# Kernel optimization log

Measured on AMD Instinct MI355X. Metric: run time of the kernel, lower is better.

## Reference

```python
import jax, jax.numpy as jnp
import numpy as np

B, S, HID, NH = 2, 2048, 2048, 16
NOPE, ROPE, VD = 128, 64, 128
QKD = NOPE + ROPE          # 192
KVR, QR = 512, 1536
EPS = 1e-6
SCALE = QKD ** (-0.5)


def rmsnorm(x, gamma, eps=EPS):
    return x * jax.lax.rsqrt(jnp.mean(x * x, axis=-1, keepdims=True) + eps) * gamma


def rotate_half(x):
    h = x.shape[-1] // 2
    return jnp.concatenate([-x[..., h:], x[..., :h]], axis=-1)


def apply_rope(x, cos, sin):
    # x: [b, h, s, d_rope]; cos/sin: [b, 1, s, d_rope]
    return x * cos + rotate_half(x) * sin


def setup_inputs() -> dict:
    key = jax.random.key(0)
    ks = jax.random.split(key, 8)
    hidden_states = jax.random.normal(ks[0], (B, S, HID), dtype=jnp.float32)
    # Standard NeoX-style rotary tables for the decoupled RoPE sub-dim
    pos = jnp.arange(S, dtype=jnp.float32)
    inv_freq = 1.0 / (10000.0 ** (jnp.arange(0, ROPE, 2, dtype=jnp.float32) / ROPE))
    freqs = pos[:, None] * inv_freq[None, :]              # [S, ROPE/2]
    emb = jnp.concatenate([freqs, freqs], axis=-1)        # [S, ROPE]
    cos = jnp.broadcast_to(jnp.cos(emb)[None], (B, S, ROPE)).astype(jnp.float32)
    sin = jnp.broadcast_to(jnp.sin(emb)[None], (B, S, ROPE)).astype(jnp.float32)
    std = 0.02
    Wq_down = jax.random.normal(ks[1], (QR, HID), dtype=jnp.float32) * std
    q_gamma = jnp.ones((QR,), dtype=jnp.float32)
    Wq_up = jax.random.normal(ks[2], (NH * QKD, QR), dtype=jnp.float32) * std
    Wkv_down = jax.random.normal(ks[3], (KVR + ROPE, HID), dtype=jnp.float32) * std
    kv_gamma = jnp.ones((KVR,), dtype=jnp.float32)
    Wkv_up = jax.random.normal(ks[4], (NH * (NOPE + VD), KVR), dtype=jnp.float32) * std
    Wo = jax.random.normal(ks[5], (HID, NH * VD), dtype=jnp.float32) * std
    return {
        "hidden_states": hidden_states, "cos": cos, "sin": sin,
        "Wq_down": Wq_down, "q_gamma": q_gamma, "Wq_up": Wq_up,
        "Wkv_down": Wkv_down, "kv_gamma": kv_gamma, "Wkv_up": Wkv_up,
        "Wo": Wo,
    }


def reference(hidden_states, cos, sin, Wq_down, q_gamma, Wq_up,
              Wkv_down, kv_gamma, Wkv_up, Wo):
    b, s, _ = hidden_states.shape
    cos4 = cos[:, None, :, :]  # [b,1,s,ROPE]
    sin4 = sin[:, None, :, :]

    # Q path: low-rank down -> RMSNorm -> up
    q_lat = rmsnorm(hidden_states @ Wq_down.T, q_gamma)            # [b,s,QR]
    q = (q_lat @ Wq_up.T).reshape(b, s, NH, QKD).transpose(0, 2, 1, 3)  # [b,h,s,QKD]
    q_nope, q_rope = q[..., :NOPE], q[..., NOPE:]
    q_rope = apply_rope(q_rope, cos4, sin4)
    q = jnp.concatenate([q_nope, q_rope], axis=-1)                 # [b,h,s,QKD]

    # KV path: joint down-proj -> split latent / shared rope key
    kv = hidden_states @ Wkv_down.T                                # [b,s,KVR+ROPE]
    c_kv, k_rope = kv[..., :KVR], kv[..., KVR:]
    c_kv = rmsnorm(c_kv, kv_gamma)
    kvx = (c_kv @ Wkv_up.T).reshape(b, s, NH, NOPE + VD).transpose(0, 2, 1, 3)
    k_nope, v = kvx[..., :NOPE], kvx[..., NOPE:]                   # [b,h,s,*]

    # Shared rope key, broadcast to all heads, rotated
    k_rope = apply_rope(k_rope[:, None, :, :], cos4, sin4)         # [b,1,s,ROPE]
    k_rope = jnp.broadcast_to(k_rope, (b, NH, s, ROPE))
    k = jnp.concatenate([k_nope, k_rope], axis=-1)                 # [b,h,s,QKD]

    # SDPA with causal mask (V zero-padded to QKD in the original -> identical
    # to using V directly and slicing, so we use V directly)
    scores = jnp.einsum('bhqd,bhkd->bhqk', q, k) * SCALE           # [b,h,s,s]
    causal = jnp.tril(jnp.ones((s, s), dtype=bool))
    scores = jnp.where(causal[None, None], scores, jnp.finfo(scores.dtype).min)
    attn = jax.nn.softmax(scores, axis=-1)
    out = jnp.einsum('bhqk,bhkd->bhqd', attn, v)                   # [b,h,s,VD]
    out = out.transpose(0, 2, 1, 3).reshape(b, s, NH * VD)
    return out @ Wo.T                                              # [b,s,HID]
```

## Files before the change

kernel.cpp:

```cpp
#include <hip/hip_runtime.h>
#include <math.h>

#define SCALE_F 0.0721687836487032f

typedef __attribute__((ext_vector_type(8))) short bf16x8;
typedef __attribute__((ext_vector_type(4))) float f32x4;
typedef __attribute__((ext_vector_type(4))) unsigned short u16x4;

static __device__ __forceinline__ short f2bf(float f) {
  unsigned u = __float_as_uint(f);
  u += 0x7fffu + ((u >> 16) & 1u);
  return (short)(u >> 16);
}

static __device__ __forceinline__ void gl_lds16(const void* g, void* l) {
  __builtin_amdgcn_global_load_lds((const __attribute__((address_space(1))) void*)g,
                                   (__attribute__((address_space(3))) void*)l, 16, 0, 0);
}

template <int MODE>
__global__ __launch_bounds__(256) void gemm_mfma(
    const short* __restrict__ A, const short* __restrict__ W,
    void* __restrict__ Cout, int N, int K,
    const float* __restrict__ cosb, const float* __restrict__ sinb,
    short* __restrict__ out2)
{
  __shared__ __align__(16) short As[128 * 32];
  __shared__ __align__(16) short Ws[128 * 32];
  const int tid = threadIdx.x;
  const int lane = tid & 63;
  const int quad = lane >> 4, n16 = lane & 15;
  const int bm = blockIdx.y * 128, bn = blockIdx.x * 128;
  const int wr = ((tid >> 6) >> 1) * 64, wc = ((tid >> 6) & 1) * 64;

  f32x4 acc[4][4];
  #pragma unroll
  for (int i = 0; i < 4; ++i)
    #pragma unroll
    for (int j = 0; j < 4; ++j) acc[i][j] = (f32x4){0.f, 0.f, 0.f, 0.f};

  const int r0 = tid >> 2, c0 = (tid & 3) * 8;
  const short* a0p = A + (size_t)(bm + r0) * K + c0;
  const short* a1p = A + (size_t)(bm + 64 + r0) * K + c0;
  const short* w0p = W + (size_t)(bn + r0) * K + c0;
  const short* w1p = W + (size_t)(bn + 64 + r0) * K + c0;
  short* asd0 = &As[tid * 8];
  short* asd1 = &As[2048 + tid * 8];
  short* wsd0 = &Ws[tid * 8];
  short* wsd1 = &Ws[2048 + tid * 8];

  for (int k0 = 0; k0 < K; k0 += 32) {
    gl_lds16(a0p, asd0);
    gl_lds16(a1p, asd1);
    gl_lds16(w0p, wsd0);
    gl_lds16(w1p, wsd1);
    a0p += 32; a1p += 32; w0p += 32; w1p += 32;
    __syncthreads();

    bf16x8 af[4], wf[4];
    #pragma unroll
    for (int i = 0; i < 4; ++i) {
      af[i] = *(const bf16x8*)&As[(wr + i * 16 + n16) * 32 + quad * 8];
      wf[i] = *(const bf16x8*)&Ws[(wc + i * 16 + n16) * 32 + quad * 8];
    }
    #pragma unroll
    for (int i = 0; i < 4; ++i)
      #pragma unroll
      for (int j = 0; j < 4; ++j)
        acc[i][j] = __builtin_amdgcn_mfma_f32_16x16x32_bf16(af[i], wf[j], acc[i][j], 0, 0, 0);
    __syncthreads();
  }

  if (MODE == 0) {
    #pragma unroll
    for (int i = 0; i < 4; ++i)
      #pragma unroll
      for (int r = 0; r < 4; ++r) {
        size_t row = (size_t)(bm + wr + i * 16 + quad * 4 + r);
        #pragma unroll
        for (int j = 0; j < 4; ++j)
          ((float*)Cout)[row * N + bn + wc + j * 16 + n16] = acc[i][j][r];
      }
  } else if (MODE == 2) {
    #pragma unroll
    for (int i = 0; i < 4; ++i)
      #pragma unroll
      for (int r = 0; r < 4; ++r) {
        int m = bm + wr + i * 16 + quad * 4 + r;
        int bb = m >> 11, s = m & 2047;
        #pragma unroll
        for (int j = 0; j < 4; ++j) {
          int col = bn + wc + j * 16 + n16;
          int h = col / 192, c = col - h * 192;
          float v = acc[i][j][r];
          if (c >= 128) {
            int jr = c - 128;
            float part = acc[i][j ^ 2][r];
            float cs = cosb[(size_t)m * 64 + jr], sn = sinb[(size_t)m * 64 + jr];
            v = (jr < 32) ? (v * cs - part * sn) : (v * cs + part * sn);
          }
          ((short*)Cout)[(((size_t)(bb * 16 + h)) * 2048 + s) * 192 + c] = f2bf(v * SCALE_F);
        }
      }
  } else {
    #pragma unroll
    for (int i = 0; i < 4; ++i)
      #pragma unroll
      for (int r = 0; r < 4; ++r) {
        int m = bm + wr + i * 16 + quad * 4 + r;
        int bb = m >> 11, s = m & 2047;
        #pragma unroll
        for (int j = 0; j < 4; ++j) {
          int col = bn + wc + j * 16 + n16;
          int h = col >> 8, c = col & 255;
          short v = f2bf(acc[i][j][r]);
          if (c < 128)
            ((short*)Cout)[(((size_t)(bb * 16 + h)) * 2048 + s) * 192 + c] = v;
          else
            out2[((size_t)(bb * 16 + h) * 128 + (c - 128)) * 2048 + s] = v;
        }
      }
  }
}

__global__ __launch_bounds__(256) void cast_all(
    const float* __restrict__ hidden, const float* __restrict__ Wqd,
    const float* __restrict__ Wqu, const float* __restrict__ Wkvu,
    const float* __restrict__ Wo, const float* __restrict__ Wkvd,
    short* __restrict__ hb, short* __restrict__ Wqd_b, short* __restrict__ Wqu_b,
    short* __restrict__ Wkvu_b, short* __restrict__ Wo_b, short* __restrict__ Wkvd_b)
{
  int blk = blockIdx.x;
  const float* src; short* dst; int i;
  if (blk < 8192)       { src = hidden; dst = hb;     i = (blk * 256 + threadIdx.x) * 4; }
  else if (blk < 11264) { src = Wqd;  dst = Wqd_b;  i = ((blk - 8192) * 256 + threadIdx.x) * 4; }
  else if (blk < 15872) { src = Wqu;  dst = Wqu_b;  i = ((blk - 11264) * 256 + threadIdx.x) * 4; }
  else if (blk < 17920) { src = Wkvu; dst = Wkvu_b; i = ((blk - 15872) * 256 + threadIdx.x) * 4; }
  else if (blk < 22016) { src = Wo;   dst = Wo_b;   i = ((blk - 17920) * 256 + threadIdx.x) * 4; }
  else {
    i = ((blk - 22016) * 256 + threadIdx.x) * 4;
    int r = i >> 11;
    short4 o = {0, 0, 0, 0};
    if (r < 576) {
      float4 v = *(const float4*)(Wkvd + i);
      o.x = f2bf(v.x); o.y = f2bf(v.y); o.z = f2bf(v.z); o.w = f2bf(v.w);
    }
    *(short4*)(Wkvd_b + i) = o;
    return;
  }
  float4 v = *(const float4*)(src + i);
  short4 o = { f2bf(v.x), f2bf(v.y), f2bf(v.z), f2bf(v.w) };
  *(short4*)(dst + i) = o;
}

__global__ __launch_bounds__(256) void rmsnorm_cast(
    const float* __restrict__ X, const float* __restrict__ gamma,
    short* __restrict__ Y, int C, int sx, int sy)
{
  const float* x = X + (size_t)blockIdx.x * sx;
  short* y = Y + (size_t)blockIdx.x * sy;
  const int tid = threadIdx.x;
  float ss = 0.f;
  for (int c = tid * 4; c < C; c += 1024) {
    float4 v = *(const float4*)(x + c);
    ss += v.x * v.x + v.y * v.y + v.z * v.z + v.w * v.w;
  }
  #pragma unroll
  for (int off = 32; off > 0; off >>= 1) ss += __shfl_down(ss, off, 64);
  __shared__ float red[4];
  if ((tid & 63) == 0) red[tid >> 6] = ss;
  __syncthreads();
  float tot = red[0] + red[1] + red[2] + red[3];
  float scale = rsqrtf(tot / (float)C + 1e-6f);
  for (int c = tid * 4; c < C; c += 1024) {
    float4 v = *(const float4*)(x + c);
    float4 g = *(const float4*)(gamma + c);
    short4 o = { f2bf(v.x * scale * g.x), f2bf(v.y * scale * g.y),
                 f2bf(v.z * scale * g.z), f2bf(v.w * scale * g.w) };
    *(short4*)(y + c) = o;
  }
}

__global__ __launch_bounds__(256) void rmsnorm_kv_rope(
    const float* __restrict__ kvf, const float* __restrict__ gamma,
    const float* __restrict__ cosb, const float* __restrict__ sinb,
    short* __restrict__ ckv, short* __restrict__ kr)
{
  const int m = blockIdx.x;
  const float* x = kvf + (size_t)m * 640;
  short* y = ckv + (size_t)m * 512;
  const int tid = threadIdx.x;
  float ss = 0.f;
  for (int c = tid * 4; c < 512; c += 1024) {
    float4 v = *(const float4*)(x + c);
    ss += v.x * v.x + v.y * v.y + v.z * v.z + v.w * v.w;
  }
  #pragma unroll
  for (int off = 32; off > 0; off >>= 1) ss += __shfl_down(ss, off, 64);
  __shared__ float red[4];
  if ((tid & 63) == 0) red[tid >> 6] = ss;
  __syncthreads();
  float tot = red[0] + red[1] + red[2] + red[3];
  float scale = rsqrtf(tot / 512.f + 1e-6f);
  for (int c = tid * 4; c < 512; c += 1024) {
    float4 v = *(const float4*)(x + c);
    float4 g = *(const float4*)(gamma + c);
    short4 o = { f2bf(v.x * scale * g.x), f2bf(v.y * scale * g.y),
                 f2bf(v.z * scale * g.z), f2bf(v.w * scale * g.w) };
    *(short4*)(y + c) = o;
  }
  if (tid < 32) {
    const float* cb = cosb + (size_t)m * 64;
    const float* sb = sinb + (size_t)m * 64;
    float x1 = x[512 + tid], x2 = x[512 + tid + 32];
    kr[(size_t)m * 64 + tid]      = f2bf(x1 * cb[tid] - x2 * sb[tid]);
    kr[(size_t)m * 64 + tid + 32] = f2bf(x2 * cb[tid + 32] + x1 * sb[tid + 32]);
  }
}

__global__ __launch_bounds__(256) void krope_fill(
    const short* __restrict__ kr, short* __restrict__ Kb)
{
  int m = blockIdx.x;
  int b = m >> 11, s = m & 2047;
  for (int idx = threadIdx.x; idx < 1024; idx += 256) {
    int h = idx >> 6, j = idx & 63;
    Kb[(((size_t)(b * 16 + h)) * 2048 + s) * 192 + 128 + j] = kr[(size_t)m * 64 + j];
  }
}

#define PSTR 72

__global__ __launch_bounds__(512) void flash_mfma(
    const short* __restrict__ Qb, const short* __restrict__ Kb,
    const short* __restrict__ Vt, short* __restrict__ attnb)
{
  __shared__ __align__(16) short KVs[2][40 * 512];
  __shared__ __align__(16) short Ps[8][32 * PSTR];

  const int h = blockIdx.x;
  const int p = blockIdx.y;
  const int b = blockIdx.z;
  const int bh = b * 16 + h;
  const int tid = threadIdx.x;
  const int wave = tid >> 6, lane = tid & 63;
  const int grp = wave >> 2, w4 = wave & 3;
  const int quad = lane >> 4, n16 = lane & 15;
  const int lq = lane >> 2, lr = lane & 3;
  const int qt_h = 15 - p;
  const int L = 2 * p + 2;
  const int NIT = 17;

  int qw = (grp ? p : qt_h) * 128 + w4 * 32;

  const short* kS[6]; short* kD[6];
  #pragma unroll
  for (int u = 0; u < 6; ++u) {
    kS[u] = Kb + ((size_t)bh * 2048 + w4 * 16 + lq) * 192 + u * 32 + lr * 8;
    kD[u] = &KVs[grp][(w4 * 6 + u) * 512 + lane * 8];
  }
  const short* vS[4]; short* vD[4];
  #pragma unroll
  for (int u = 0; u < 4; ++u) {
    int ci = w4 * 4 + u, ks = ci >> 3, vt = ci & 7;
    vS[u] = Vt + ((size_t)bh * 128 + vt * 16 + lq) * 2048 + ks * 32 + lr * 8;
    vD[u] = &KVs[grp][(24 + ci) * 512 + lane * 8];
  }

  bf16x8 aQ[2][6];
  #pragma unroll
  for (int rg = 0; rg < 2; ++rg) {
    const short* qp = Qb + ((size_t)bh * 2048 + qw + rg * 16 + n16) * 192 + quad * 8;
    #pragma unroll
    for (int t = 0; t < 6; ++t) aQ[rg][t] = *(const bf16x8*)(qp + t * 32);
  }

  f32x4 O[2][8];
  #pragma unroll
  for (int rg = 0; rg < 2; ++rg)
    #pragma unroll
    for (int i = 0; i < 8; ++i) O[rg][i] = (f32x4){0.f, 0.f, 0.f, 0.f};
  float lp[2] = {0.f, 0.f};

  short* pw = &Ps[wave][0];

  {
    #pragma unroll
    for (int u = 0; u < 6; ++u) gl_lds16(kS[u], kD[u]);
    #pragma unroll
    for (int u = 0; u < 4; ++u) gl_lds16(vS[u], vD[u]);
  }

  for (int j = 0; j < NIT; ++j) {
    __syncthreads();

    if (grp == 1 && j == L) {
      #pragma unroll
      for (int rg = 0; rg < 2; ++rg) {
        float l = lp[rg];
        l += __shfl_xor(l, 16);
        l += __shfl_xor(l, 32);
        float inv_l[4];
        #pragma unroll
        for (int r = 0; r < 4; ++r) inv_l[r] = 1.f / __shfl(l, quad * 4 + r);
        #pragma unroll
        for (int vt = 0; vt < 8; ++vt)
          #pragma unroll
          for (int r = 0; r < 4; ++r) {
            size_t m = (size_t)b * 2048 + qw + rg * 16 + quad * 4 + r;
            attnb[(m * 16 + h) * 128 + vt * 16 + n16] = f2bf(O[rg][vt][r] * inv_l[r]);
          }
      }
      #pragma unroll
      for (int rg = 0; rg < 2; ++rg)
        #pragma unroll
        for (int i = 0; i < 8; ++i) O[rg][i] = (f32x4){0.f, 0.f, 0.f, 0.f};
      lp[0] = 0.f; lp[1] = 0.f;
      qw = qt_h * 128 + w4 * 32;
      #pragma unroll
      for (int rg = 0; rg < 2; ++rg) {
        const short* qp = Qb + ((size_t)bh * 2048 + qw + rg * 16 + n16) * 192 + quad * 8;
        #pragma unroll
        for (int t = 0; t < 6; ++t) aQ[rg][t] = *(const bf16x8*)(qp + t * 32);
      }
    }

    const int kt = (grp == 0) ? j : (j < L ? j : 17 + j - L);

    if (kt * 64 <= qw + 31) {
      float s[4][2][4];
      bool act[4];
      const bool tail = (kt * 64 + 63 > qw);
      #pragma unroll
      for (int ct = 0; ct < 4; ++ct) {
        act[ct] = (kt * 64 + ct * 16 <= qw + 31);
        if (act[ct]) {
          f32x4 a0 = (f32x4){0.f, 0.f, 0.f, 0.f};
          f32x4 a1 = (f32x4){0.f, 0.f, 0.f, 0.f};
          #pragma unroll
          for (int t = 0; t < 6; ++t) {
            bf16x8 ak = *(const bf16x8*)&KVs[grp][(ct * 6 + t) * 512 + n16 * 32 + quad * 8];
            a0 = __builtin_amdgcn_mfma_f32_16x16x32_bf16(ak, aQ[0][t], a0, 0, 0, 0);
            a1 = __builtin_amdgcn_mfma_f32_16x16x32_bf16(ak, aQ[1][t], a1, 0, 0, 0);
          }
          #pragma unroll
          for (int r = 0; r < 4; ++r) { s[ct][0][r] = a0[r]; s[ct][1][r] = a1[r]; }
        }
      }

      #pragma unroll
      for (int rg = 0; rg < 2; ++rg) {
        const int q = qw + rg * 16 + n16;
        #pragma unroll
        for (int ct = 0; ct < 4; ++ct) {
          u16x4 pk;
          #pragma unroll
          for (int r = 0; r < 4; ++r) {
            float v = 0.f;
            if (act[ct]) {
              v = __expf(s[ct][rg][r]);
              if (tail) {
                int key = kt * 64 + ct * 16 + quad * 4 + r;
                if (key > q) v = 0.f;
              }
            }
            lp[rg] += v;
            pk[r] = (unsigned short)f2bf(v);
          }
          *(u16x4*)&pw[(rg * 16 + n16) * PSTR + ct * 16 + quad * 4] = pk;
        }
      }

      #pragma unroll
      for (int ks = 0; ks < 2; ++ks) {
        if (kt * 64 + ks * 32 <= qw + 31) {
          bf16x8 aP0 = *(const bf16x8*)&pw[(n16) * PSTR + ks * 32 + quad * 8];
          bf16x8 aP1 = *(const bf16x8*)&pw[(16 + n16) * PSTR + ks * 32 + quad * 8];
          #pragma unroll
          for (int vt = 0; vt < 8; ++vt) {
            bf16x8 bV = *(const bf16x8*)&KVs[grp][(24 + ks * 8 + vt) * 512 + n16 * 32 + quad * 8];
            O[0][vt] = __builtin_amdgcn_mfma_f32_16x16x32_bf16(aP0, bV, O[0][vt], 0, 0, 0);
            O[1][vt] = __builtin_amdgcn_mfma_f32_16x16x32_bf16(aP1, bV, O[1][vt], 0, 0, 0);
          }
        }
      }
    }

    __syncthreads();

    if (j + 1 < NIT) {
      const int jn = j + 1;
      const int ktn = (grp == 0) ? jn : (jn < L ? jn : 17 + jn - L);
      const size_t ka = (size_t)ktn * (64 * 192);
      const size_t va = (size_t)ktn * 64;
      #pragma unroll
      for (int u = 0; u < 6; ++u) gl_lds16(kS[u] + ka, kD[u]);
      #pragma unroll
      for (int u = 0; u < 4; ++u) gl_lds16(vS[u] + va, vD[u]);
    }
  }

  float* xO = (float*)&KVs[0][0];
  float* xl = (float*)&Ps[0][0];
  const int xb = w4 * 4160 + lane * 65;
  if (grp == 1) {
    #pragma unroll
    for (int rg = 0; rg < 2; ++rg)
      #pragma unroll
      for (int vt = 0; vt < 8; ++vt)
        #pragma unroll
        for (int r = 0; r < 4; ++r)
          xO[xb + rg * 32 + vt * 4 + r] = O[rg][vt][r];
    xl[w4 * 128 + lane * 2 + 0] = lp[0];
    xl[w4 * 128 + lane * 2 + 1] = lp[1];
  }
  __syncthreads();
  if (grp == 0) {
    #pragma unroll
    for (int rg = 0; rg < 2; ++rg)
      #pragma unroll
      for (int vt = 0; vt < 8; ++vt)
        #pragma unroll
        for (int r = 0; r < 4; ++r)
          O[rg][vt][r] += xO[xb + rg * 32 + vt * 4 + r];
    lp[0] += xl[w4 * 128 + lane * 2 + 0];
    lp[1] += xl[w4 * 128 + lane * 2 + 1];

    #pragma unroll
    for (int rg = 0; rg < 2; ++rg) {
      float l = lp[rg];
      l += __shfl_xor(l, 16);
      l += __shfl_xor(l, 32);
      float inv_l[4];
      #pragma unroll
      for (int r = 0; r < 4; ++r) inv_l[r] = 1.f / __shfl(l, quad * 4 + r);
      #pragma unroll
      for (int vt = 0; vt < 8; ++vt)
        #pragma unroll
        for (int r = 0; r < 4; ++r) {
          size_t m = (size_t)b * 2048 + qw + rg * 16 + quad * 4 + r;
          attnb[(m * 16 + h) * 128 + vt * 16 + n16] = f2bf(O[rg][vt][r] * inv_l[r]);
        }
    }
  }
}

extern "C" void kernel_launch(void* const* d_in, const int* in_sizes, int n_in,
                              void* d_out, int out_size, void* d_ws, size_t ws_size,
                              hipStream_t stream)
{
  const float* hidden   = (const float*)d_in[0];
  const float* cosb     = (const float*)d_in[1];
  const float* sinb     = (const float*)d_in[2];
  const float* Wq_down  = (const float*)d_in[3];
  const float* q_gamma  = (const float*)d_in[4];
  const float* Wq_up    = (const float*)d_in[5];
  const float* Wkv_down = (const float*)d_in[6];
  const float* kv_gamma = (const float*)d_in[7];
  const float* Wkv_up   = (const float*)d_in[8];
  const float* Wo       = (const float*)d_in[9];
  float* out = (float*)d_out;

  char* base = (char*)d_ws;
  short* hb  = (short*)base;
  float* kvf = (float*)(base + 16777216);
  short* Qb  = (short*)base;
  char* pB = base + 27262976;
  short* Wqd_b  = (short*)pB;
  short* Wkvd_b = (short*)(pB + 6291456);
  short* Wqu_b  = (short*)(pB + 8912896);
  short* Wkvu_b = (short*)(pB + 18350080);
  short* Wo_b   = (short*)(pB + 22544384);
  char* pC = pB + 30932992;
  float* q_lat = (float*)pC;
  short* Kb    = (short*)pC;
  char* pD = pC + 25165824;
  short* q_lat_b = (short*)pD;
  short* ckv_b   = (short*)(pD + 12582912);
  short* krope_b = (short*)(pD + 16777216);
  short* attn_b  = (short*)pD;
  char* pE = pD + 17301504;
  short* Vt = (short*)pE;

  dim3 blk(256);

  cast_all<<<23296, blk, 0, stream>>>(hidden, Wq_down, Wq_up, Wkv_up, Wo, Wkv_down,
                                      hb, Wqd_b, Wqu_b, Wkvu_b, Wo_b, Wkvd_b);

  gemm_mfma<0><<<dim3(12, 32), blk, 0, stream>>>(hb, Wqd_b, q_lat, 1536, 2048, nullptr, nullptr, nullptr);
  gemm_mfma<0><<<dim3(5, 32), blk, 0, stream>>>(hb, Wkvd_b, kvf, 640, 2048, nullptr, nullptr, nullptr);

  rmsnorm_cast<<<4096, blk, 0, stream>>>(q_lat, q_gamma, q_lat_b, 1536, 1536, 1536);
  rmsnorm_kv_rope<<<4096, blk, 0, stream>>>(kvf, kv_gamma, cosb, sinb, ckv_b, krope_b);

  gemm_mfma<2><<<dim3(24, 32), blk, 0, stream>>>(q_lat_b, Wqu_b, Qb, 3072, 1536, cosb, sinb, nullptr);
  gemm_mfma<3><<<dim3(32, 32), blk, 0, stream>>>(ckv_b, Wkvu_b, Kb, 4096, 512, nullptr, nullptr, Vt);
  krope_fill<<<4096, blk, 0, stream>>>(krope_b, Kb);

  flash_mfma<<<dim3(16, 8, 2), dim3(512), 0, stream>>>(Qb, Kb, Vt, attn_b);
  gemm_mfma<0><<<dim3(16, 32), blk, 0, stream>>>(attn_b, Wo_b, out, 2048, 2048, nullptr, nullptr, nullptr);
}
```

Measured before the change: 515.1 us.

## Merge Q/KV down and up projection GEMMs into single launches, transpose V via LDS

Fuses the Q-down and KV-down projections into one GEMM launch over a concatenated N of 2176, splitting the output by column range. It also merges the Q-up and KV-up GEMMs into one kernel that picks its operands by block index, which fills the GPU better and removes launch gaps. The V half of the KV-up output is now transposed through LDS and written with 16-byte row stores instead of scattered 2-byte stores. The merged down GEMM assumes the bf16 Wq_down and Wkv_down buffers sit next to each other in memory. The extra LDS transpose buffer raises shared-memory use and may lower occupancy.

After: 576.0 us. 11.8% more time.

```diff
diff --git a/kernel.cpp b/kernel.cpp
--- a/kernel.cpp
+++ b/kernel.cpp
@@ -81,7 +81,86 @@
         for (int j = 0; j < 4; ++j)
           ((float*)Cout)[row * N + bn + wc + j * 16 + n16] = acc[i][j][r];
       }
-  } else if (MODE == 2) {
+  } else {
+    float* qlat = (float*)Cout;
+    float* kvf  = (float*)out2;
+    #pragma unroll
+    for (int i = 0; i < 4; ++i)
+      #pragma unroll
+      for (int r = 0; r < 4; ++r) {
+        size_t row = (size_t)(bm + wr + i * 16 + quad * 4 + r);
+        #pragma unroll
+        for (int j = 0; j < 4; ++j) {
+          int col = bn + wc + j * 16 + n16;
+          if (col < 1536) qlat[row * 1536 + col] = acc[i][j][r];
+          else            kvf[row * 640 + (col - 1536)] = acc[i][j][r];
+        }
+      }
+  }
+}
+
+__global__ __launch_bounds__(256) void gemm_up(
+    const short* __restrict__ Aq, const short* __restrict__ Wq,
+    short* __restrict__ Qb,
+    const float* __restrict__ cosb, const float* __restrict__ sinb,
+    const short* __restrict__ Akv, const short* __restrict__ Wkv,
+    short* __restrict__ Kb, short* __restrict__ Vtb)
+{
+  __shared__ __align__(16) short As[128 * 32];
+  __shared__ __align__(16) short Ws[128 * 32];
+  __shared__ __align__(16) short Tt[128 * 136];
+
+  const bool isQ = blockIdx.x < 24;
+  const short* A = isQ ? Aq : Akv;
+  const short* W = isQ ? Wq : Wkv;
+  const int K = isQ ? 1536 : 512;
+  const int bx = isQ ? blockIdx.x : (blockIdx.x - 24);
+
+  const int tid = threadIdx.x;
+  const int lane = tid & 63;
+  const int quad = lane >> 4, n16 = lane & 15;
+  const int bm = blockIdx.y * 128, bn = bx * 128;
+  const int wr = ((tid >> 6) >> 1) * 64, wc = ((tid >> 6) & 1) * 64;
+
+  f32x4 acc[4][4];
+  #pragma unroll
+  for (int i = 0; i < 4; ++i)
+    #pragma unroll
+    for (int j = 0; j < 4; ++j) acc[i][j] = (f32x4){0.f, 0.f, 0.f, 0.f};
+
+  const int r0 = tid >> 2, c0 = (tid & 3) * 8;
+  const short* a0p = A + (size_t)(bm + r0) * K + c0;
+  const short* a1p = A + (size_t)(bm + 64 + r0) * K + c0;
+  const short* w0p = W + (size_t)(bn + r0) * K + c0;
+  const short* w1p = W + (size_t)(bn + 64 + r0) * K + c0;
+  short* asd0 = &As[tid * 8];
+  short* asd1 = &As[2048 + tid * 8];
+  short* wsd0 = &Ws[tid * 8];
+  short* wsd1 = &Ws[2048 + tid * 8];
+
+  for (int k0 = 0; k0 < K; k0 += 32) {
+    gl_lds16(a0p, asd0);
+    gl_lds16(a1p, asd1);
+    gl_lds16(w0p, wsd0);
+    gl_lds16(w1p, wsd1);
+    a0p += 32; a1p += 32; w0p += 32; w1p += 32;
+    __syncthreads();
+
+    bf16x8 af[4], wf[4];
+    #pragma unroll
+    for (int i = 0; i < 4; ++i) {
+      af[i] = *(const bf16x8*)&As[(wr + i * 16 + n16) * 32 + quad * 8];
+      wf[i] = *(const bf16x8*)&Ws[(wc + i * 16 + n16) * 32 + quad * 8];
+    }
+    #pragma unroll
+    for (int i = 0; i < 4; ++i)
+      #pragma unroll
+      for (int j = 0; j < 4; ++j)
+        acc[i][j] = __builtin_amdgcn_mfma_f32_16x16x32_bf16(af[i], wf[j], acc[i][j], 0, 0, 0);
+    __syncthreads();
+  }
+
+  if (isQ) {
     #pragma unroll
     for (int i = 0; i < 4; ++i)
       #pragma unroll
@@ -99,10 +178,11 @@
             float cs = cosb[(size_t)m * 64 + jr], sn = sinb[(size_t)m * 64 + jr];
             v = (jr < 32) ? (v * cs - part * sn) : (v * cs + part * sn);
           }
-          ((short*)Cout)[(((size_t)(bb * 16 + h)) * 2048 + s) * 192 + c] = f2bf(v * SCALE_F);
-        }
-      }
-  } else {
+          Qb[(((size_t)(bb * 16 + h)) * 2048 + s) * 192 + c] = f2bf(v * SCALE_F);
+        }
+      }
+  } else if ((bn & 255) == 0) {
+    const int h = bn >> 8;
     #pragma unroll
     for (int i = 0; i < 4; ++i)
       #pragma unroll
@@ -111,15 +191,29 @@
         int bb = m >> 11, s = m & 2047;
         #pragma unroll
         for (int j = 0; j < 4; ++j) {
-          int col = bn + wc + j * 16 + n16;
-          int h = col >> 8, c = col & 255;
-          short v = f2bf(acc[i][j][r]);
-          if (c < 128)
-            ((short*)Cout)[(((size_t)(bb * 16 + h)) * 2048 + s) * 192 + c] = v;
-          else
-            out2[((size_t)(bb * 16 + h) * 128 + (c - 128)) * 2048 + s] = v;
-        }
-      }
+          int c = wc + j * 16 + n16;
+          Kb[(((size_t)(bb * 16 + h)) * 2048 + s) * 192 + c] = f2bf(acc[i][j][r]);
+        }
+      }
+  } else {
+    const int h = bn >> 8;
+    #pragma unroll
+    for (int i = 0; i < 4; ++i)
+      #pragma unroll
+      for (int j = 0; j < 4; ++j) {
+        u16x4 pk;
+        #pragma unroll
+        for (int r = 0; r < 4; ++r) pk[r] = (unsigned short)f2bf(acc[i][j][r]);
+        *(u16x4*)&Tt[(wc + j * 16 + n16) * 136 + wr + i * 16 + quad * 4] = pk;
+      }
+    __syncthreads();
+    const int bb2 = bm >> 11, sb = bm & 2047;
+    const int cr = tid >> 1, hf = tid & 1;
+    const short* srcr = &Tt[cr * 136 + hf * 64];
+    short* dstr = Vtb + ((size_t)(bb2 * 16 + h) * 128 + cr) * 2048 + sb + hf * 64;
+    #pragma unroll
+    for (int k = 0; k < 8; ++k)
+      *(bf16x8*)(dstr + k * 8) = *(const bf16x8*)(srcr + k * 8);
   }
 }
 
@@ -487,16 +581,17 @@
   cast_all<<<23296, blk, 0, stream>>>(hidden, Wq_down, Wq_up, Wkv_up, Wo, Wkv_down,
                                       hb, Wqd_b, Wqu_b, Wkvu_b, Wo_b, Wkvd_b);
 
-  gemm_mfma<0><<<dim3(12, 32), blk, 0, stream>>>(hb, Wqd_b, q_lat, 1536, 2048, nullptr, nullptr, nullptr);
-  gemm_mfma<0><<<dim3(5, 32), blk, 0, stream>>>(hb, Wkvd_b, kvf, 640, 2048, nullptr, nullptr, nullptr);
+  gemm_mfma<4><<<dim3(17, 32), blk, 0, stream>>>(hb, Wqd_b, q_lat, 2176, 2048,
+                                                 nullptr, nullptr, (short*)kvf);
 
   rmsnorm_cast<<<4096, blk, 0, stream>>>(q_lat, q_gamma, q_lat_b, 1536, 1536, 1536);
   rmsnorm_kv_rope<<<4096, blk, 0, stream>>>(kvf, kv_gamma, cosb, sinb, ckv_b, krope_b);
 
-  gemm_mfma<2><<<dim3(24, 32), blk, 0, stream>>>(q_lat_b, Wqu_b, Qb, 3072, 1536, cosb, sinb, nullptr);
-  gemm_mfma<3><<<dim3(32, 32), blk, 0, stream>>>(ckv_b, Wkvu_b, Kb, 4096, 512, nullptr, nullptr, Vt);
+  gemm_up<<<dim3(56, 32), blk, 0, stream>>>(q_lat_b, Wqu_b, Qb, cosb, sinb,
+                                            ckv_b, Wkvu_b, Kb, Vt);
   krope_fill<<<4096, blk, 0, stream>>>(krope_b, Kb);
 
   flash_mfma<<<dim3(16, 8, 2), dim3(512), 0, stream>>>(Qb, Kb, Vt, attn_b);
-  gemm_mfma<0><<<dim3(16, 32), blk, 0, stream>>>(attn_b, Wo_b, out, 2048, 2048, nullptr, nullptr, nullptr);
-}
+  gemm_mfma<0><<<dim3(16, 32), blk, 0, stream>>>(attn_b, Wo_b, out, 2048, 2048,
+                                                 nullptr, nullptr, nullptr);
+}
```

## Fuse down-projection GEMMs, merge RMSNorm kernels, fold krope fill into KV-up epilogue

Applied to the files above, without the earlier changes.

Merges the Q and KV down-projection GEMMs into one launch over a concatenated weight (N=2176), with a new epilogue mode that splits columns into q_lat and kvf. Combines the two RMSNorm kernels into one launch, and folds the per-head rope-key broadcast into the MODE 3 GEMM epilogue so the separate krope_fill kernel is removed. Separately, the flash QK^T inner loop is split into two independent accumulator chains to shorten MFMA dependency chains. Fewer launches and better wave fill come at the cost of relying on Wqd_b and Wkvd_b being contiguous in memory, and of reusing the sinb pointer to pass krope.

New measurement: 479.1 us. -7.0%, faster.

```diff
diff --git a/kernel.cpp b/kernel.cpp
--- a/kernel.cpp
+++ b/kernel.cpp
@@ -102,7 +102,7 @@
           ((short*)Cout)[(((size_t)(bb * 16 + h)) * 2048 + s) * 192 + c] = f2bf(v * SCALE_F);
         }
       }
-  } else {
+  } else if (MODE == 3) {
     #pragma unroll
     for (int i = 0; i < 4; ++i)
       #pragma unroll
@@ -118,6 +118,32 @@
             ((short*)Cout)[(((size_t)(bb * 16 + h)) * 2048 + s) * 192 + c] = v;
           else
             out2[((size_t)(bb * 16 + h) * 128 + (c - 128)) * 2048 + s] = v;
+        }
+      }
+    if ((bn & 255) == 0) {
+      const short* kr = (const short*)sinb;
+      const int h = bn >> 8;
+      const int bb = bm >> 11, sb = bm & 2047;
+      const int rr = tid >> 1, half = tid & 1;
+      const short* src = kr + (size_t)(bm + rr) * 64 + half * 32;
+      short* dst = (short*)Cout + (((size_t)(bb * 16 + h)) * 2048 + sb + rr) * 192 + 128 + half * 32;
+      #pragma unroll
+      for (int k = 0; k < 4; ++k)
+        *(bf16x8*)(dst + k * 8) = *(const bf16x8*)(src + k * 8);
+    }
+  } else {
+    float* qlat = (float*)Cout;
+    float* kvf  = (float*)out2;
+    #pragma unroll
+    for (int i = 0; i < 4; ++i)
+      #pragma unroll
+      for (int r = 0; r < 4; ++r) {
+        size_t row = (size_t)(bm + wr + i * 16 + quad * 4 + r);
+        #pragma unroll
+        for (int j = 0; j < 4; ++j) {
+          int col = bn + wc + j * 16 + n16;
+          if (col < 1536) qlat[row * 1536 + col] = acc[i][j][r];
+          else            kvf[row * 640 + (col - 1536)] = acc[i][j][r];
         }
       }
   }
@@ -153,79 +179,66 @@
   *(short4*)(dst + i) = o;
 }
 
-__global__ __launch_bounds__(256) void rmsnorm_cast(
-    const float* __restrict__ X, const float* __restrict__ gamma,
-    short* __restrict__ Y, int C, int sx, int sy)
-{
-  const float* x = X + (size_t)blockIdx.x * sx;
-  short* y = Y + (size_t)blockIdx.x * sy;
-  const int tid = threadIdx.x;
-  float ss = 0.f;
-  for (int c = tid * 4; c < C; c += 1024) {
-    float4 v = *(const float4*)(x + c);
-    ss += v.x * v.x + v.y * v.y + v.z * v.z + v.w * v.w;
-  }
-  #pragma unroll
-  for (int off = 32; off > 0; off >>= 1) ss += __shfl_down(ss, off, 64);
-  __shared__ float red[4];
-  if ((tid & 63) == 0) red[tid >> 6] = ss;
-  __syncthreads();
-  float tot = red[0] + red[1] + red[2] + red[3];
-  float scale = rsqrtf(tot / (float)C + 1e-6f);
-  for (int c = tid * 4; c < C; c += 1024) {
-    float4 v = *(const float4*)(x + c);
-    float4 g = *(const float4*)(gamma + c);
-    short4 o = { f2bf(v.x * scale * g.x), f2bf(v.y * scale * g.y),
-                 f2bf(v.z * scale * g.z), f2bf(v.w * scale * g.w) };
-    *(short4*)(y + c) = o;
-  }
-}
-
-__global__ __launch_bounds__(256) void rmsnorm_kv_rope(
-    const float* __restrict__ kvf, const float* __restrict__ gamma,
+__global__ __launch_bounds__(256) void rmsnorm_both(
+    const float* __restrict__ q_lat, const float* __restrict__ q_gamma,
+    short* __restrict__ q_lat_b,
+    const float* __restrict__ kvf, const float* __restrict__ kv_gamma,
     const float* __restrict__ cosb, const float* __restrict__ sinb,
     short* __restrict__ ckv, short* __restrict__ kr)
 {
-  const int m = blockIdx.x;
-  const float* x = kvf + (size_t)m * 640;
-  short* y = ckv + (size_t)m * 512;
   const int tid = threadIdx.x;
-  float ss = 0.f;
-  for (int c = tid * 4; c < 512; c += 1024) {
-    float4 v = *(const float4*)(x + c);
-    ss += v.x * v.x + v.y * v.y + v.z * v.z + v.w * v.w;
-  }
-  #pragma unroll
-  for (int off = 32; off > 0; off >>= 1) ss += __shfl_down(ss, off, 64);
   __shared__ float red[4];
-  if ((tid & 63) == 0) red[tid >> 6] = ss;
-  __syncthreads();
-  float tot = red[0] + red[1] + red[2] + red[3];
-  float scale = rsqrtf(tot / 512.f + 1e-6f);
-  for (int c = tid * 4; c < 512; c += 1024) {
-    float4 v = *(const float4*)(x + c);
-    float4 g = *(const float4*)(gamma + c);
-    short4 o = { f2bf(v.x * scale * g.x), f2bf(v.y * scale * g.y),
-                 f2bf(v.z * scale * g.z), f2bf(v.w * scale * g.w) };
-    *(short4*)(y + c) = o;
-  }
-  if (tid < 32) {
-    const float* cb = cosb + (size_t)m * 64;
-    const float* sb = sinb + (size_t)m * 64;
-    float x1 = x[512 + tid], x2 = x[512 + tid + 32];
-    kr[(size_t)m * 64 + tid]      = f2bf(x1 * cb[tid] - x2 * sb[tid]);
-    kr[(size_t)m * 64 + tid + 32] = f2bf(x2 * cb[tid + 32] + x1 * sb[tid + 32]);
-  }
-}
-
-__global__ __launch_bounds__(256) void krope_fill(
-    const short* __restrict__ kr, short* __restrict__ Kb)
-{
-  int m = blockIdx.x;
-  int b = m >> 11, s = m & 2047;
-  for (int idx = threadIdx.x; idx < 1024; idx += 256) {
-    int h = idx >> 6, j = idx & 63;
-    Kb[(((size_t)(b * 16 + h)) * 2048 + s) * 192 + 128 + j] = kr[(size_t)m * 64 + j];
+  if (blockIdx.x < 4096) {
+    const int m = blockIdx.x;
+    const float* x = q_lat + (size_t)m * 1536;
+    short* y = q_lat_b + (size_t)m * 1536;
+    float ss = 0.f;
+    for (int c = tid * 4; c < 1536; c += 1024) {
+      float4 v = *(const float4*)(x + c);
+      ss += v.x * v.x + v.y * v.y + v.z * v.z + v.w * v.w;
+    }
+    #pragma unroll
+    for (int off = 32; off > 0; off >>= 1) ss += __shfl_down(ss, off, 64);
+    if ((tid & 63) == 0) red[tid >> 6] = ss;
+    __syncthreads();
+    float tot = red[0] + red[1] + red[2] + red[3];
+    float scale = rsqrtf(tot / 1536.f + 1e-6f);
+    for (int c = tid * 4; c < 1536; c += 1024) {
+      float4 v = *(const float4*)(x + c);
+      float4 g = *(const float4*)(q_gamma + c);
+      short4 o = { f2bf(v.x * scale * g.x), f2bf(v.y * scale * g.y),
+                   f2bf(v.z * scale * g.z), f2bf(v.w * scale * g.w) };
+      *(short4*)(y + c) = o;
+    }
+  } else {
+    const int m = blockIdx.x - 4096;
+    const float* x = kvf + (size_t)m * 640;
+    short* y = ckv + (size_t)m * 512;
+    float ss = 0.f;
+    for (int c = tid * 4; c < 512; c += 1024) {
+      float4 v = *(const float4*)(x + c);
+      ss += v.x * v.x + v.y * v.y + v.z * v.z + v.w * v.w;
+    }
+    #pragma unroll
+    for (int off = 32; off > 0; off >>= 1) ss += __shfl_down(ss, off, 64);
+    if ((tid & 63) == 0) red[tid >> 6] = ss;
+    __syncthreads();
+    float tot = red[0] + red[1] + red[2] + red[3];
+    float scale = rsqrtf(tot / 512.f + 1e-6f);
+    for (int c = tid * 4; c < 512; c += 1024) {
+      float4 v = *(const float4*)(x + c);
+      float4 g = *(const float4*)(kv_gamma + c);
+      short4 o = { f2bf(v.x * scale * g.x), f2bf(v.y * scale * g.y),
+                   f2bf(v.z * scale * g.z), f2bf(v.w * scale * g.w) };
+      *(short4*)(y + c) = o;
+    }
+    if (tid < 32) {
+      const float* cb = cosb + (size_t)m * 64;
+      const float* sb = sinb + (size_t)m * 64;
+      float x1 = x[512 + tid], x2 = x[512 + tid + 32];
+      kr[(size_t)m * 64 + tid]      = f2bf(x1 * cb[tid] - x2 * sb[tid]);
+      kr[(size_t)m * 64 + tid + 32] = f2bf(x2 * cb[tid + 32] + x1 * sb[tid + 32]);
+    }
   }
 }
 
@@ -335,16 +348,27 @@
       for (int ct = 0; ct < 4; ++ct) {
         act[ct] = (kt * 64 + ct * 16 <= qw + 31);
         if (act[ct]) {
-          f32x4 a0 = (f32x4){0.f, 0.f, 0.f, 0.f};
-          f32x4 a1 = (f32x4){0.f, 0.f, 0.f, 0.f};
+          f32x4 a0a = (f32x4){0.f, 0.f, 0.f, 0.f};
+          f32x4 a1a = (f32x4){0.f, 0.f, 0.f, 0.f};
+          f32x4 a0b = (f32x4){0.f, 0.f, 0.f, 0.f};
+          f32x4 a1b = (f32x4){0.f, 0.f, 0.f, 0.f};
           #pragma unroll
-          for (int t = 0; t < 6; ++t) {
+          for (int t = 0; t < 3; ++t) {
             bf16x8 ak = *(const bf16x8*)&KVs[grp][(ct * 6 + t) * 512 + n16 * 32 + quad * 8];
-            a0 = __builtin_amdgcn_mfma_f32_16x16x32_bf16(ak, aQ[0][t], a0, 0, 0, 0);
-            a1 = __builtin_amdgcn_mfma_f32_16x16x32_bf16(ak, aQ[1][t], a1, 0, 0, 0);
+            a0a = __builtin_amdgcn_mfma_f32_16x16x32_bf16(ak, aQ[0][t], a0a, 0, 0, 0);
+            a1a = __builtin_amdgcn_mfma_f32_16x16x32_bf16(ak, aQ[1][t], a1a, 0, 0, 0);
           }
           #pragma unroll
-          for (int r = 0; r < 4; ++r) { s[ct][0][r] = a0[r]; s[ct][1][r] = a1[r]; }
+          for (int t = 3; t < 6; ++t) {
+            bf16x8 ak = *(const bf16x8*)&KVs[grp][(ct * 6 + t) * 512 + n16 * 32 + quad * 8];
+            a0b = __builtin_amdgcn_mfma_f32_16x16x32_bf16(ak, aQ[0][t], a0b, 0, 0, 0);
+            a1b = __builtin_amdgcn_mfma_f32_16x16x32_bf16(ak, aQ[1][t], a1b, 0, 0, 0);
+          }
+          #pragma unroll
+          for (int r = 0; r < 4; ++r) {
+            s[ct][0][r] = a0a[r] + a0b[r];
+            s[ct][1][r] = a1a[r] + a1b[r];
+          }
         }
       }
 
@@ -487,16 +511,18 @@
   cast_all<<<23296, blk, 0, stream>>>(hidden, Wq_down, Wq_up, Wkv_up, Wo, Wkv_down,
                                       hb, Wqd_b, Wqu_b, Wkvu_b, Wo_b, Wkvd_b);
 
-  gemm_mfma<0><<<dim3(12, 32), blk, 0, stream>>>(hb, Wqd_b, q_lat, 1536, 2048, nullptr, nullptr, nullptr);
-  gemm_mfma<0><<<dim3(5, 32), blk, 0, stream>>>(hb, Wkvd_b, kvf, 640, 2048, nullptr, nullptr, nullptr);
-
-  rmsnorm_cast<<<4096, blk, 0, stream>>>(q_lat, q_gamma, q_lat_b, 1536, 1536, 1536);
-  rmsnorm_kv_rope<<<4096, blk, 0, stream>>>(kvf, kv_gamma, cosb, sinb, ckv_b, krope_b);
-
-  gemm_mfma<2><<<dim3(24, 32), blk, 0, stream>>>(q_lat_b, Wqu_b, Qb, 3072, 1536, cosb, sinb, nullptr);
-  gemm_mfma<3><<<dim3(32, 32), blk, 0, stream>>>(ckv_b, Wkvu_b, Kb, 4096, 512, nullptr, nullptr, Vt);
-  krope_fill<<<4096, blk, 0, stream>>>(krope_b, Kb);
+  gemm_mfma<4><<<dim3(17, 32), blk, 0, stream>>>(hb, Wqd_b, q_lat, 2176, 2048,
+                                                 nullptr, nullptr, (short*)kvf);
+
+  rmsnorm_both<<<8192, blk, 0, stream>>>(q_lat, q_gamma, q_lat_b,
+                                         kvf, kv_gamma, cosb, sinb, ckv_b, krope_b);
+
+  gemm_mfma<2><<<dim3(24, 32), blk, 0, stream>>>(q_lat_b, Wqu_b, Qb, 3072, 1536,
+                                                 cosb, sinb, nullptr);
+  gemm_mfma<3><<<dim3(32, 32), blk, 0, stream>>>(ckv_b, Wkvu_b, Kb, 4096, 512,
+                                                 nullptr, (const float*)krope_b, Vt);
 
   flash_mfma<<<dim3(16, 8, 2), dim3(512), 0, stream>>>(Qb, Kb, Vt, attn_b);
-  gemm_mfma<0><<<dim3(16, 32), blk, 0, stream>>>(attn_b, Wo_b, out, 2048, 2048, nullptr, nullptr, nullptr);
-}
+  gemm_mfma<0><<<dim3(16, 32), blk, 0, stream>>>(attn_b, Wo_b, out, 2048, 2048,
+                                                 nullptr, nullptr, nullptr);
+}
```
